# Kernel optimization log

Measured on AMD Instinct MI355X. Metric: run time of the kernel, lower is better.

Reference implementation:

```python
import jax, jax.numpy as jnp
import numpy as np

B, C, T = 32, 64, 512
K = 3            # period_channels / top-k frequencies
PMAX = T         # max period (== seq_len so output matches input length)
MIN_P = 32       # min_period_threshold
CMAX = T // MIN_P  # static upper bound on number of cycles
KERNELS = ((1, 1), (3, 3), (5, 5))


def _conv2d(x, w, b, pad):
    # x: [N, Cin, H, W], w: [Cout, Cin, kh, kw]
    y = jax.lax.conv_general_dilated(
        x, w, (1, 1), ((pad[0], pad[0]), (pad[1], pad[1])),
        dimension_numbers=('NCHW', 'OIHW', 'NCHW'))
    return y + b[None, :, None, None]


def _period_fold(seqs):
    # seqs: [BN, T]. FFT top-k period detection + gather-based fold into 2D grids.
    spec = jnp.fft.rfft(seqs, axis=-1)
    amp = jnp.abs(spec).at[..., 0].set(0.0)  # zero DC component
    vals, idx = jax.lax.top_k(amp, K)        # [BN, K]
    idx = jnp.maximum(idx, 1)
    P = jnp.clip(T // idx, MIN_P, PMAX)      # period length per branch
    cycles = jnp.maximum(T // P, 1)
    base = jnp.maximum(T - cycles * P, 0)    # start offset (keep trailing window)
    idx_c = jnp.arange(CMAX)
    idx_p = jnp.arange(PMAX)
    gidx = (base[:, :, None, None]
            + idx_c[None, None, :, None] * P[:, :, None, None]
            + idx_p[None, None, None, :])
    gidx = jnp.clip(gidx, 0, T - 1)          # [BN, K, CMAX, PMAX]
    gathered = seqs[jnp.arange(seqs.shape[0])[:, None, None, None], gidx]
    mask = ((idx_c[None, None, :, None] < cycles[:, :, None, None])
            & (idx_p[None, None, None, :] < P[:, :, None, None])).astype(seqs.dtype)
    return gathered * mask, mask, vals


def _forward(features, w_path0, b_path0, w_path1, b_path1, w_path2, b_path2,
             w_proj, b_proj, w_res, b_res, w_fuse, b_fuse):
    seqs = features.reshape(B * C, T)
    conv_in, mask, kamp = _period_fold(seqs)  # [B*C, K, CMAX, PMAX]
    # Inception block: parallel same-padded convs + 1x1 proj + residual 1x1 proj
    ws = (w_path0, w_path1, w_path2)
    bs = (b_path0, b_path1, b_path2)
    feats = [_conv2d(conv_in, w, b, (kh // 2, kw // 2))
             for w, b, (kh, kw) in zip(ws, bs, KERNELS)]
    z = _conv2d(jnp.concatenate(feats, axis=1), w_proj, b_proj, (0, 0))
    z = jax.nn.gelu(z, approximate=False)  # torch nn.GELU default = exact erf
    z2d = (z + _conv2d(conv_in, w_res, b_res, (0, 0))).reshape(B, C, CMAX, PMAX)
    mask5 = mask.reshape(B, C, K, CMAX, PMAX)
    conv_in5 = conv_in.reshape(B, C, K, CMAX, PMAX)
    eps = jnp.finfo(z2d.dtype).eps
    neg = jnp.finfo(z2d.dtype).min
    # masked avg / max pooling over cycles
    cycle_mask = mask5.max(axis=2)                       # [B,C,CMAX,PMAX]
    avg_pool = (z2d * cycle_mask).sum(axis=2) / (cycle_mask.sum(axis=2) + eps)
    valid = cycle_mask > 0
    max_pool = jnp.where(valid, z2d, neg).max(axis=2)
    max_pool = jnp.where(valid.any(axis=2), max_pool, 0.0)  # [B,C,PMAX]
    # amplitude-softmax weighted branch reconstruction back to 1D
    branch_sum = conv_in5.sum(axis=3)                    # [B,C,K,PMAX]
    branch_w = mask5.sum(axis=3)
    branch_recon = branch_sum / (branch_w + eps) * (branch_w > 0)
    branch_valid = mask5.max(axis=(3, 4)) > 0            # [B,C,K]
    amp = jnp.where(branch_valid, kamp.reshape(B, C, K), neg)
    bw = jax.nn.softmax(amp, axis=2) * branch_valid
    seq_recon = (branch_recon * bw[..., None]).sum(axis=2)  # [B,C,PMAX]
    combined = jnp.concatenate([avg_pool, max_pool, seq_recon], axis=1)  # [B,3C,PMAX]
    fused = jnp.einsum('oc,bct->bot', w_fuse, combined) + b_fuse[None, :, None]
    return jax.nn.gelu(fused, approximate=False)  # [B, C, T] residual update


def setup_inputs() -> dict:
    key = jax.random.key(0)
    ks = jax.random.split(key, 8)

    def conv_w(k, shape):
        fan_in = shape[1] * shape[2] * shape[3]
        return jax.random.normal(k, shape, jnp.float32) / float(np.sqrt(fan_in))

    inp = {'features': jax.random.normal(ks[0], (B, C, T), jnp.float32)}
    for i, (kh, kw) in enumerate(KERNELS):
        inp[f'w_path{i}'] = conv_w(ks[1 + i], (1, K, kh, kw))
        inp[f'b_path{i}'] = jnp.zeros((1,), jnp.float32)
    inp['w_proj'] = conv_w(ks[4], (1, len(KERNELS), 1, 1))
    inp['b_proj'] = jnp.zeros((1,), jnp.float32)
    inp['w_res'] = conv_w(ks[5], (1, K, 1, 1))
    inp['b_res'] = jnp.zeros((1,), jnp.float32)
    inp['w_fuse'] = jax.random.normal(ks[6], (C, 3 * C), jnp.float32) / float(np.sqrt(3 * C))
    inp['b_fuse'] = jnp.zeros((C,), jnp.float32)
    return inp


def reference(features, w_path0, b_path0, w_path1, b_path1, w_path2, b_path2,
              w_proj, b_proj, w_res, b_res, w_fuse, b_fuse):
    return _forward(features, w_path0, b_path0, w_path1, b_path1, w_path2, b_path2,
                    w_proj, b_proj, w_res, b_res, w_fuse, b_fuse)
```

## Files before the change

### kernel.cpp

```cpp
#include <hip/hip_runtime.h>
#include <math.h>

#define B_    32
#define C_    64
#define T_    512
#define NROWS (B_ * C_)
#define CMAX_ 16
#define FEPS  1.1920929e-07f

__device__ __forceinline__ float gelu_fast(float x) {
    float y = fmaf(0.044715f * x * x, x, x);
    float e = __builtin_exp2f(-2.3022808f * y);
    return x * __builtin_amdgcn_rcpf(1.0f + e);
}

__global__ __launch_bounds__(128) void mono_kernel(
    const float* __restrict__ feat,
    const float* __restrict__ w0, const float* __restrict__ b0,
    const float* __restrict__ w1, const float* __restrict__ b1,
    const float* __restrict__ w2, const float* __restrict__ b2,
    const float* __restrict__ wpj, const float* __restrict__ bpj,
    const float* __restrict__ wr, const float* __restrict__ br,
    float* __restrict__ avg_out, float* __restrict__ max_out,
    float* __restrict__ seq_out)
{
    __shared__ float rowp[1040];
    __shared__ __align__(16) float2 FA[256];
    __shared__ __align__(16) float2 FB[256];
    __shared__ float WeffS[80];
    __shared__ float wtopS[6];
    __shared__ int   itopS[6];
    __shared__ int   ipS[9];
    __shared__ float bwS[3];

    const int tid = threadIdx.x;
    const int lane = tid & 63;
    const int wv = tid >> 6;
    const int r = blockIdx.x;

    {
        float4 v = reinterpret_cast<const float4*>(feat + (size_t)r * T_)[tid];
        int bi = 2 + tid * 4;
        rowp[bi + 0] = v.x; rowp[bi + 1] = v.y;
        rowp[bi + 2] = v.z; rowp[bi + 3] = v.w;
    }
    for (int i = 514 + tid; i < 1040; i += 128) rowp[i] = 0.f;
    if (tid == 0) { rowp[0] = 0.f; rowp[1] = 0.f; }
    if (tid < 80) {
        int i = tid;
        if (i < 75) {
            int k = i / 25, ij = i % 25, ii = ij / 5, jj = ij % 5;
            float w = wpj[2] * w2[k * 25 + ii * 5 + jj];
            if (ii >= 1 && ii <= 3 && jj >= 1 && jj <= 3)
                w += wpj[1] * w1[k * 9 + (ii - 1) * 3 + (jj - 1)];
            if (ii == 2 && jj == 2) w += wpj[0] * w0[k];
            WeffS[i] = w;
        } else if (i == 75) {
            WeffS[75] = wpj[0] * b0[0] + wpj[1] * b1[0] + wpj[2] * b2[0] + bpj[0];
        } else if (i <= 78) {
            WeffS[i] = wr[i - 76];
        } else {
            WeffS[79] = br[0];
        }
    }
    __syncthreads();

    {
        float2* Fw = FA + (wv << 7);
        #pragma unroll
        for (int n = lane; n < 128; n += 64)
            Fw[n] = make_float2(rowp[2 + 4 * n + 2 * wv], rowp[3 + 4 * n + 2 * wv]);
    }

    {
        float2* src = FA + (wv << 7);
        float2* dst = FB + (wv << 7);
        #pragma unroll
        for (int s = 1; s <= 7; ++s) {
            const int l = 1 << (s - 1);
            const int pl = lane & (l - 1);
            const int i0 = 2 * lane - pl;
            const float rev = (float)pl * (0.5f / (float)l);
            const float cw =  __builtin_amdgcn_cosf(rev);
            const float sw = -__builtin_amdgcn_sinf(rev);
            float2 a = src[lane];
            float2 b = src[lane + 64];
            float tr = cw * b.x - sw * b.y;
            float ti = cw * b.y + sw * b.x;
            dst[i0]     = make_float2(a.x + tr, a.y + ti);
            dst[i0 + l] = make_float2(a.x - tr, a.y - ti);
            float2* tmp = src; src = dst; dst = tmp;
        }
    }
    __syncthreads();

    float v[2]; int id[2];
    {
        const float2* Fe = FB;
        const float2* Fo = FB + 128;
        const int k1 = tid + 1;
        const int a = k1 & 127;
        const int b = (128 - a) & 127;
        float2 Fea = Fe[a], Foa = Fo[a], Feb = Fe[b], Fob = Fo[b];
        const float revw = (float)k1 * (1.0f / 256.0f);
        const float cw =  __builtin_amdgcn_cosf(revw);
        const float sw = -__builtin_amdgcn_sinf(revw);
        float wfr = cw * Foa.x - sw * Foa.y, wfi = cw * Foa.y + sw * Foa.x;
        float cfr = cw * Fob.x + sw * Fob.y, cfi = cw * Fob.y - sw * Fob.x;
        const float revu = (float)k1 * (1.0f / 512.0f);
        const float su = __builtin_amdgcn_sinf(revu);
        const float cu = __builtin_amdgcn_cosf(revu);
        #pragma unroll
        for (int q = 0; q < 2; ++q) {
            const float sgn = q ? -1.f : 1.f;
            float Ax = Fea.x + sgn * wfr, Ay = Fea.y + sgn * wfi;
            float Bx = Feb.x + sgn * cfr, By = Feb.y + sgn * cfi;
            float Er = 0.5f * (Ax + Bx);
            float Ei = 0.5f * (Ay - By);
            float Or = 0.5f * (Ay + By);
            float Oi = 0.5f * (Bx - Ax);
            float cth = q ? -su : cu;
            float sth = q ?  cu : su;
            float Fr = Er + cth * Or + sth * Oi;
            float Fi = Ei + cth * Oi - sth * Or;
            v[q] = sqrtf(Fr * Fr + Fi * Fi);
            id[q] = k1 + 128 * q;
        }
    }

    {
        float vals[3]; int idxs[3];
        #pragma unroll
        for (int kk = 0; kk < 3; ++kk) {
            float bv = v[0]; int bi = id[0];
            if (v[1] > bv || (v[1] == bv && id[1] < bi)) { bv = v[1]; bi = id[1]; }
            #pragma unroll
            for (int off = 32; off >= 1; off >>= 1) {
                float ov = __shfl_xor(bv, off, 64);
                int   oi = __shfl_xor(bi, off, 64);
                if (ov > bv || (ov == bv && oi < bi)) { bv = ov; bi = oi; }
            }
            vals[kk] = bv; idxs[kk] = bi;
            #pragma unroll
            for (int q = 0; q < 2; ++q)
                if (id[q] == bi) v[q] = -1e30f;
        }
        if (lane == 0) {
            #pragma unroll
            for (int kk = 0; kk < 3; ++kk) {
                wtopS[wv * 3 + kk] = vals[kk];
                itopS[wv * 3 + kk] = idxs[kk];
            }
        }
    }
    __syncthreads();
    if (tid == 0) {
        float vv[6]; int ii[6];
        #pragma unroll
        for (int q = 0; q < 6; ++q) { vv[q] = wtopS[q]; ii[q] = itopS[q]; }
        float vals[3]; int idxs[3];
        #pragma unroll
        for (int kk = 0; kk < 3; ++kk) {
            float bv = vv[0]; int bi = ii[0];
            #pragma unroll
            for (int q = 1; q < 6; ++q)
                if (vv[q] > bv || (vv[q] == bv && ii[q] < bi)) { bv = vv[q]; bi = ii[q]; }
            vals[kk] = bv; idxs[kk] = bi;
            #pragma unroll
            for (int q = 0; q < 6; ++q)
                if (ii[q] == bi) vv[q] = -1e30f;
        }
        float m = fmaxf(vals[0], fmaxf(vals[1], vals[2]));
        float e0 = expf(vals[0] - m), e1 = expf(vals[1] - m), e2 = expf(vals[2] - m);
        float inv = 1.0f / (e0 + e1 + e2);
        bwS[0] = e0 * inv; bwS[1] = e1 * inv; bwS[2] = e2 * inv;
        #pragma unroll
        for (int kk = 0; kk < 3; ++kk) {
            int fi = idxs[kk];
            int P = T_ / fi;
            P = P < 32 ? 32 : (P > 512 ? 512 : P);
            int cyc = T_ / P;
            ipS[kk] = P; ipS[3 + kk] = cyc; ipS[6 + kk] = T_ - cyc * P;
        }
    }
    __syncthreads();

    const int P0  = __builtin_amdgcn_readfirstlane(ipS[0]);
    const int P1  = __builtin_amdgcn_readfirstlane(ipS[1]);
    const int P2  = __builtin_amdgcn_readfirstlane(ipS[2]);
    const int cy0 = __builtin_amdgcn_readfirstlane(ipS[3]);
    const int cy1 = __builtin_amdgcn_readfirstlane(ipS[4]);
    const int cy2 = __builtin_amdgcn_readfirstlane(ipS[5]);
    const int bs0 = __builtin_amdgcn_readfirstlane(ipS[6]);
    const int bs1 = __builtin_amdgcn_readfirstlane(ipS[7]);
    const int bs2 = __builtin_amdgcn_readfirstlane(ipS[8]);
    const float bw0 = bwS[0], bw1 = bwS[1], bw2 = bwS[2];
    const float beff = WeffS[75], wr0 = WeffS[76], wr1 = WeffS[77],
                wr2 = WeffS[78], bres = WeffS[79];

    int maxP = P0 > P1 ? P0 : P1; maxP = maxP > P2 ? maxP : P2;
    const int PkA[3]  = {P0, P1, P2};
    const int cykA[3] = {cy0, cy1, cy2};
    const int bskA[3] = {bs0, bs1, bs2};
    const int woff = tid & 64;

    #pragma unroll 1
    for (int pc = 0; pc < T_; pc += 128) {
        const int p = pc + tid;
        const int wb = __builtin_amdgcn_readfirstlane(pc + woff);
        if (wb >= maxP) {
            avg_out[r * T_ + p] = 0.f;
            max_out[r * T_ + p] = 0.f;
            seq_out[r * T_ + p] = 0.f;
            continue;
        }
        int c0 = (P0 > wb) ? cy0 : 0;
        int c1 = (P1 > wb) ? cy1 : 0;
        int c2 = (P2 > wb) ? cy2 : 0;
        int cymax = c0 > c1 ? c0 : c1; cymax = cymax > c2 ? cymax : c2;
        cymax = __builtin_amdgcn_readfirstlane(cymax);

        float zacc[CMAX_];
        #pragma unroll
        for (int i = 0; i < CMAX_; ++i) zacc[i] = beff;

        #pragma unroll 1
        for (int k = 0; k < 3; ++k) {
            const int P = PkA[k];
            if (wb >= P) continue;
            const int cy = cykA[k];
            const int bs = bskA[k];
            float Wk[5][5];
            #pragma unroll
            for (int i = 0; i < 5; ++i)
                #pragma unroll
                for (int j = 0; j < 5; ++j)
                    Wk[i][j] = WeffS[k * 25 + i * 5 + j];
            bool mdw[5];
            #pragma unroll
            for (int dw = -2; dw <= 2; ++dw)
                mdw[dw + 2] = ((unsigned)(p + dw) < (unsigned)P);
            const int base = bs + p;
            #pragma unroll
            for (int g = 0; g < 4; ++g) {
                if (4 * g < cy) {
                    #pragma unroll
                    for (int h4 = 0; h4 < 4; ++h4) {
                        const int hh = 4 * g + h4;
                        const int hoff = (hh < cy) ? 0 : 4096;
                        int a0 = base + hh * P + hoff;
                        a0 = a0 > 1031 ? 1031 : a0;
                        float w[5];
                        #pragma unroll
                        for (int dw = 0; dw < 5; ++dw)
                            w[dw] = mdw[dw] ? rowp[a0 + dw] : 0.f;
                        #pragma unroll
                        for (int dh = -2; dh <= 2; ++dh) {
                            const int cc = hh - dh;
                            if (cc >= 0 && cc < CMAX_) {
                                #pragma unroll
                                for (int dw = 0; dw < 5; ++dw)
                                    zacc[cc] = fmaf(Wk[dh + 2][dw], w[dw], zacc[cc]);
                            }
                        }
                    }
                }
            }
        }

        float avg_num = 0.f, den = 0.f, mx = -3.402823466e38f;
        float s0 = 0.f, s1 = 0.f, s2 = 0.f;
        int anyv = 0;
        const int pl0 = (p < P0), pl1 = (p < P1), pl2 = (p < P2);
        #pragma unroll
        for (int cg = 0; cg < 4; ++cg) {
            if (4 * cg < cymax) {
                #pragma unroll
                for (int c4 = 0; c4 < 4; ++c4) {
                    const int cc = 4 * cg + c4;
                    int m0 = (cc < cy0) & pl0;
                    int m1 = (cc < cy1) & pl1;
                    int m2 = (cc < cy2) & pl2;
                    int a0 = 2 + bs0 + cc * P0 + p; a0 = a0 > 1036 ? 1036 : a0;
                    int a1 = 2 + bs1 + cc * P1 + p; a1 = a1 > 1036 ? 1036 : a1;
                    int a2 = 2 + bs2 + cc * P2 + p; a2 = a2 > 1036 ? 1036 : a2;
                    float x0v = m0 ? rowp[a0] : 0.f;
                    float x1v = m1 ? rowp[a1] : 0.f;
                    float x2v = m2 ? rowp[a2] : 0.f;
                    float res = fmaf(wr0, x0v, fmaf(wr1, x1v, fmaf(wr2, x2v, bres)));
                    float z = gelu_fast(zacc[cc]) + res;
                    s0 += x0v; s1 += x1v; s2 += x2v;
                    int mm = m0 | m1 | m2;
                    float cm = mm ? 1.f : 0.f;
                    avg_num += z * cm;
                    den += cm;
                    mx = mm ? fmaxf(mx, z) : mx;
                    anyv |= mm;
                }
            }
        }
        float avg = avg_num / (den + FEPS);
        float mpool = anyv ? mx : 0.f;

        float seq = 0.f;
        seq = fmaf(bw0, pl0 ? s0 / ((float)cy0 + FEPS) : 0.f, seq);
        seq = fmaf(bw1, pl1 ? s1 / ((float)cy1 + FEPS) : 0.f, seq);
        seq = fmaf(bw2, pl2 ? s2 / ((float)cy2 + FEPS) : 0.f, seq);

        avg_out[r * T_ + p] = avg;
        max_out[r * T_ + p] = mpool;
        seq_out[r * T_ + p] = seq;
    }
}

__global__ __launch_bounds__(256) void fuse_kernel(
    const float* __restrict__ avgb, const float* __restrict__ maxb,
    const float* __restrict__ seqb,
    const float* __restrict__ wf, const float* __restrict__ bfu,
    float* __restrict__ out)
{
    __shared__ float wT[64][70];
    __shared__ float Bt[64][40];
    const int tid = threadIdx.x;
    const int b = blockIdx.y;
    const int tt0 = blockIdx.x * 32;
    const int og = tid >> 3;
    const int tg = tid & 7;
    const int o0 = og * 2;
    const int t0 = tg * 4;

    float acc[2][4];
    #pragma unroll
    for (int i = 0; i < 2; ++i)
        #pragma unroll
        for (int j = 0; j < 4; ++j) acc[i][j] = 0.f;

    const float* srcs[3] = {avgb, maxb, seqb};
    for (int g = 0; g < 3; ++g) {
        const float* __restrict__ src = srcs[g];
        #pragma unroll
        for (int it = 0; it < 2; ++it) {
            int idx = tid + it * 256;
            int c = idx >> 3, t4 = idx & 7;
            float4 vv = reinterpret_cast<const float4*>(
                            &src[(b * 64 + c) * 512 + tt0])[t4];
            *reinterpret_cast<float4*>(&Bt[c][t4 * 4]) = vv;
        }
        #pragma unroll
        for (int it = 0; it < 16; ++it) {
            int i = tid + it * 256;
            int c = i & 63, o = i >> 6;
            wT[c][o] = wf[o * 192 + g * 64 + c];
        }
        __syncthreads();
        for (int c = 0; c < 64; ++c) {
            float2 wv = *reinterpret_cast<const float2*>(&wT[c][o0]);
            float4 bv = *reinterpret_cast<const float4*>(&Bt[c][t0]);
            const float wa[2] = {wv.x, wv.y};
            const float ba[4] = {bv.x, bv.y, bv.z, bv.w};
            #pragma unroll
            for (int i = 0; i < 2; ++i)
                #pragma unroll
                for (int j = 0; j < 4; ++j)
                    acc[i][j] = fmaf(wa[i], ba[j], acc[i][j]);
        }
        __syncthreads();
    }
    #pragma unroll
    for (int i = 0; i < 2; ++i) {
        float bias = bfu[o0 + i];
        float4 o4;
        o4.x = gelu_fast(acc[i][0] + bias);
        o4.y = gelu_fast(acc[i][1] + bias);
        o4.z = gelu_fast(acc[i][2] + bias);
        o4.w = gelu_fast(acc[i][3] + bias);
        *reinterpret_cast<float4*>(
            &out[(b * 64 + (o0 + i)) * 512 + tt0 + t0]) = o4;
    }
}

extern "C" void kernel_launch(void* const* d_in, const int* in_sizes, int n_in,
                              void* d_out, int out_size, void* d_ws, size_t ws_size,
                              hipStream_t stream) {
    const float* feat = (const float*)d_in[0];
    const float* w0  = (const float*)d_in[1];
    const float* b0  = (const float*)d_in[2];
    const float* w1  = (const float*)d_in[3];
    const float* b1  = (const float*)d_in[4];
    const float* w2  = (const float*)d_in[5];
    const float* b2  = (const float*)d_in[6];
    const float* wpj = (const float*)d_in[7];
    const float* bpj = (const float*)d_in[8];
    const float* wr  = (const float*)d_in[9];
    const float* br  = (const float*)d_in[10];
    const float* wf  = (const float*)d_in[11];
    const float* bfu = (const float*)d_in[12];

    float* ws = (float*)d_ws;
    float* avgb = ws;
    float* maxb = ws + (size_t)NROWS * T_;
    float* seqb = ws + 2 * (size_t)NROWS * T_;

    mono_kernel<<<NROWS, 128, 0, stream>>>(feat, w0, b0, w1, b1, w2, b2,
                                           wpj, bpj, wr, br, avgb, maxb, seqb);
    fuse_kernel<<<dim3(16, 32), 256, 0, stream>>>(avgb, maxb, seqb, wf, bfu,
                                                  (float*)d_out);
}
```

Baseline: 41.11 us.

## Restructure fold-conv as flattened shared-memory scatter over valid cycle×period cells

Replaces the per-thread register accumulation over all 16 cycle rows with a pass that flattens the valid (cycle, period) cells across threads and writes conv results into a shared-memory z tile, processed in two 256-wide column windows. When all three branch periods match, the three effective 5x5 kernels are summed into one so a single conv pass runs. The z tile reuses the FFT scratch buffers, and the padded row buffer shrinks. The pooling loop becomes a runtime loop bounded by the actual cycle count. This is meant to cut wasted FMAs on masked cells and register pressure, at the cost of extra barriers, shared-memory traffic and a reciprocal-multiply index division.

```diff
diff --git a/kernel.cpp b/kernel.cpp
--- a/kernel.cpp
+++ b/kernel.cpp
@@ -5,13 +5,52 @@
 #define C_    64
 #define T_    512
 #define NROWS (B_ * C_)
-#define CMAX_ 16
 #define FEPS  1.1920929e-07f
+#define ZSTR  260
 
 __device__ __forceinline__ float gelu_fast(float x) {
     float y = fmaf(0.044715f * x * x, x, x);
     float e = __builtin_exp2f(-2.3022808f * y);
     return x * __builtin_amdgcn_rcpf(1.0f + e);
+}
+
+template<bool ACC>
+__device__ __forceinline__ void conv_pass(
+    const float* __restrict__ rowp, float* __restrict__ zsm,
+    const float Wk[5][5], int P, int cy, int bs,
+    int cyI, int PI, int w, int tid)
+{
+    int PwI = PI - (w << 8);
+    PwI = PwI > 256 ? 256 : PwI;
+    if (PwI <= 0) return;
+    const int n = cyI * PwI;
+    const unsigned M = 0xFFFFFFFFu / (unsigned)PwI + 1u;
+    for (int i = tid; i < n; i += 128) {
+        const int cc  = (int)(((unsigned long long)(unsigned)i * M) >> 32);
+        const int ppw = i - cc * PwI;
+        const int pp  = ppw + (w << 8);
+        const int rb  = bs + cc * P + pp;
+        bool hv[5], qv[5];
+        #pragma unroll
+        for (int d = 0; d < 5; ++d) {
+            hv[d] = (unsigned)(cc + d - 2) < (unsigned)cy;
+            qv[d] = (unsigned)(pp + d - 2) < (unsigned)P;
+        }
+        float acc = 0.f;
+        #pragma unroll
+        for (int dh = 0; dh < 5; ++dh) {
+            const int ra = rb + (dh - 2) * P;
+            #pragma unroll
+            for (int dw = 0; dw < 5; ++dw) {
+                unsigned a = (unsigned)(ra + dw - 2);
+                a = a > 511u ? 511u : a;
+                float val = (hv[dh] && qv[dw]) ? rowp[2 + a] : 0.f;
+                acc = fmaf(Wk[dh][dw], val, acc);
+            }
+        }
+        float* zp = zsm + cc * ZSTR + ppw;
+        if (ACC) *zp += acc; else *zp = acc;
+    }
 }
 
 __global__ __launch_bounds__(128) void mono_kernel(
@@ -24,14 +63,16 @@
     float* __restrict__ avg_out, float* __restrict__ max_out,
     float* __restrict__ seq_out)
 {
-    __shared__ float rowp[1040];
-    __shared__ __align__(16) float2 FA[256];
-    __shared__ __align__(16) float2 FB[256];
+    __shared__ float rowp[520];
     __shared__ float WeffS[80];
     __shared__ float wtopS[6];
     __shared__ int   itopS[6];
     __shared__ int   ipS[9];
     __shared__ float bwS[3];
+    __shared__ __align__(16) float smem_u[16 * ZSTR];
+    float2* FA = reinterpret_cast<float2*>(smem_u);
+    float2* FB = FA + 256;
+    float*  zsm = smem_u;
 
     const int tid = threadIdx.x;
     const int lane = tid & 63;
@@ -44,8 +85,8 @@
         rowp[bi + 0] = v.x; rowp[bi + 1] = v.y;
         rowp[bi + 2] = v.z; rowp[bi + 3] = v.w;
     }
-    for (int i = 514 + tid; i < 1040; i += 128) rowp[i] = 0.f;
-    if (tid == 0) { rowp[0] = 0.f; rowp[1] = 0.f; }
+    if (tid < 2) rowp[tid] = 0.f;
+    if (tid >= 122) rowp[392 + tid] = 0.f;
     if (tid < 80) {
         int i = tid;
         if (i < 75) {
@@ -199,117 +240,99 @@
                 wr2 = WeffS[78], bres = WeffS[79];
 
     int maxP = P0 > P1 ? P0 : P1; maxP = maxP > P2 ? maxP : P2;
+    const bool fastp = (P0 == P1) && (P1 == P2);
     const int PkA[3]  = {P0, P1, P2};
     const int cykA[3] = {cy0, cy1, cy2};
     const int bskA[3] = {bs0, bs1, bs2};
-    const int woff = tid & 64;
+    const size_t rT = (size_t)r * T_;
 
     #pragma unroll 1
-    for (int pc = 0; pc < T_; pc += 128) {
-        const int p = pc + tid;
-        const int wb = __builtin_amdgcn_readfirstlane(pc + woff);
-        if (wb >= maxP) {
-            avg_out[r * T_ + p] = 0.f;
-            max_out[r * T_ + p] = 0.f;
-            seq_out[r * T_ + p] = 0.f;
-            continue;
-        }
-        int c0 = (P0 > wb) ? cy0 : 0;
-        int c1 = (P1 > wb) ? cy1 : 0;
-        int c2 = (P2 > wb) ? cy2 : 0;
-        int cymax = c0 > c1 ? c0 : c1; cymax = cymax > c2 ? cymax : c2;
-        cymax = __builtin_amdgcn_readfirstlane(cymax);
-
-        float zacc[CMAX_];
-        #pragma unroll
-        for (int i = 0; i < CMAX_; ++i) zacc[i] = beff;
+    for (int w = 0; w < 2; ++w) {
+        const int wbase = w << 8;
+        if (wbase < maxP) {
+            if (fastp) {
+                float Wk[5][5];
+                #pragma unroll
+                for (int ij = 0; ij < 25; ++ij)
+                    (&Wk[0][0])[ij] = WeffS[ij] + WeffS[25 + ij] + WeffS[50 + ij];
+                conv_pass<false>(rowp, zsm, Wk, P0, cy0, bs0, cy0, P0, w, tid);
+                __syncthreads();
+            } else {
+                #pragma unroll
+                for (int j = 0; j < 8; ++j) {
+                    int idx = tid + (j << 7);
+                    int cc = idx >> 6, p4 = idx & 63;
+                    *reinterpret_cast<float4*>(zsm + cc * ZSTR + (p4 << 2)) =
+                        make_float4(0.f, 0.f, 0.f, 0.f);
+                }
+                __syncthreads();
+                #pragma unroll 1
+                for (int k = 0; k < 3; ++k) {
+                    float Wk[5][5];
+                    #pragma unroll
+                    for (int ij = 0; ij < 25; ++ij)
+                        (&Wk[0][0])[ij] = WeffS[k * 25 + ij];
+                    const int P = PkA[k], cyk = cykA[k], bsk = bskA[k];
+                    int cyI = cyk + 2; cyI = cyI > 16 ? 16 : cyI;
+                    int PI  = P + 2;   PI  = PI > 512 ? 512 : PI;
+                    conv_pass<true>(rowp, zsm, Wk, P, cyk, bsk, cyI, PI, w, tid);
+                    __syncthreads();
+                }
+            }
+        }
 
         #pragma unroll 1
-        for (int k = 0; k < 3; ++k) {
-            const int P = PkA[k];
-            if (wb >= P) continue;
-            const int cy = cykA[k];
-            const int bs = bskA[k];
-            float Wk[5][5];
-            #pragma unroll
-            for (int i = 0; i < 5; ++i)
-                #pragma unroll
-                for (int j = 0; j < 5; ++j)
-                    Wk[i][j] = WeffS[k * 25 + i * 5 + j];
-            bool mdw[5];
-            #pragma unroll
-            for (int dw = -2; dw <= 2; ++dw)
-                mdw[dw + 2] = ((unsigned)(p + dw) < (unsigned)P);
-            const int base = bs + p;
-            #pragma unroll
-            for (int g = 0; g < 4; ++g) {
-                if (4 * g < cy) {
-                    #pragma unroll
-                    for (int h4 = 0; h4 < 4; ++h4) {
-                        const int hh = 4 * g + h4;
-                        const int hoff = (hh < cy) ? 0 : 4096;
-                        int a0 = base + hh * P + hoff;
-                        a0 = a0 > 1031 ? 1031 : a0;
-                        float w[5];
-                        #pragma unroll
-                        for (int dw = 0; dw < 5; ++dw)
-                            w[dw] = mdw[dw] ? rowp[a0 + dw] : 0.f;
-                        #pragma unroll
-                        for (int dh = -2; dh <= 2; ++dh) {
-                            const int cc = hh - dh;
-                            if (cc >= 0 && cc < CMAX_) {
-                                #pragma unroll
-                                for (int dw = 0; dw < 5; ++dw)
-                                    zacc[cc] = fmaf(Wk[dh + 2][dw], w[dw], zacc[cc]);
-                            }
-                        }
-                    }
-                }
-            }
-        }
-
-        float avg_num = 0.f, den = 0.f, mx = -3.402823466e38f;
-        float s0 = 0.f, s1 = 0.f, s2 = 0.f;
-        int anyv = 0;
-        const int pl0 = (p < P0), pl1 = (p < P1), pl2 = (p < P2);
-        #pragma unroll
-        for (int cg = 0; cg < 4; ++cg) {
-            if (4 * cg < cymax) {
-                #pragma unroll
-                for (int c4 = 0; c4 < 4; ++c4) {
-                    const int cc = 4 * cg + c4;
-                    int m0 = (cc < cy0) & pl0;
-                    int m1 = (cc < cy1) & pl1;
-                    int m2 = (cc < cy2) & pl2;
-                    int a0 = 2 + bs0 + cc * P0 + p; a0 = a0 > 1036 ? 1036 : a0;
-                    int a1 = 2 + bs1 + cc * P1 + p; a1 = a1 > 1036 ? 1036 : a1;
-                    int a2 = 2 + bs2 + cc * P2 + p; a2 = a2 > 1036 ? 1036 : a2;
-                    float x0v = m0 ? rowp[a0] : 0.f;
-                    float x1v = m1 ? rowp[a1] : 0.f;
-                    float x2v = m2 ? rowp[a2] : 0.f;
-                    float res = fmaf(wr0, x0v, fmaf(wr1, x1v, fmaf(wr2, x2v, bres)));
-                    float z = gelu_fast(zacc[cc]) + res;
-                    s0 += x0v; s1 += x1v; s2 += x2v;
-                    int mm = m0 | m1 | m2;
-                    float cm = mm ? 1.f : 0.f;
-                    avg_num += z * cm;
-                    den += cm;
-                    mx = mm ? fmaxf(mx, z) : mx;
-                    anyv |= mm;
-                }
-            }
-        }
-        float avg = avg_num / (den + FEPS);
-        float mpool = anyv ? mx : 0.f;
-
-        float seq = 0.f;
-        seq = fmaf(bw0, pl0 ? s0 / ((float)cy0 + FEPS) : 0.f, seq);
-        seq = fmaf(bw1, pl1 ? s1 / ((float)cy1 + FEPS) : 0.f, seq);
-        seq = fmaf(bw2, pl2 ? s2 / ((float)cy2 + FEPS) : 0.f, seq);
-
-        avg_out[r * T_ + p] = avg;
-        max_out[r * T_ + p] = mpool;
-        seq_out[r * T_ + p] = seq;
+        for (int half = 0; half < 2; ++half) {
+            const int pc = wbase + (half << 7);
+            const int p = pc + tid;
+            if (pc >= maxP) {
+                avg_out[rT + p] = 0.f;
+                max_out[rT + p] = 0.f;
+                seq_out[rT + p] = 0.f;
+                continue;
+            }
+            int c0 = (P0 > pc) ? cy0 : 0;
+            int c1 = (P1 > pc) ? cy1 : 0;
+            int c2 = (P2 > pc) ? cy2 : 0;
+            int cymaxc = c0 > c1 ? c0 : c1; cymaxc = cymaxc > c2 ? cymaxc : c2;
+
+            float avg_num = 0.f, den = 0.f, mx = -3.402823466e38f;
+            float s0 = 0.f, s1 = 0.f, s2 = 0.f;
+            int anyv = 0;
+            const int pl0 = (p < P0), pl1 = (p < P1), pl2 = (p < P2);
+            #pragma unroll 1
+            for (int cc = 0; cc < cymaxc; ++cc) {
+                int m0 = (cc < cy0) & pl0;
+                int m1 = (cc < cy1) & pl1;
+                int m2 = (cc < cy2) & pl2;
+                float zr = zsm[cc * ZSTR + (p - wbase)];
+                unsigned a0 = (unsigned)(bs0 + cc * P0 + p); a0 = a0 > 511u ? 511u : a0;
+                unsigned a1 = (unsigned)(bs1 + cc * P1 + p); a1 = a1 > 511u ? 511u : a1;
+                unsigned a2 = (unsigned)(bs2 + cc * P2 + p); a2 = a2 > 511u ? 511u : a2;
+                float x0v = m0 ? rowp[2 + a0] : 0.f;
+                float x1v = m1 ? rowp[2 + a1] : 0.f;
+                float x2v = m2 ? rowp[2 + a2] : 0.f;
+                float res = fmaf(wr0, x0v, fmaf(wr1, x1v, fmaf(wr2, x2v, bres)));
+                float zv = gelu_fast(zr + beff) + res;
+                int mm = m0 | m1 | m2;
+                avg_num += mm ? zv : 0.f;
+                den     += mm ? 1.f : 0.f;
+                mx = mm ? fmaxf(mx, zv) : mx;
+                anyv |= mm;
+                s0 += x0v; s1 += x1v; s2 += x2v;
+            }
+            float avg = avg_num / (den + FEPS);
+            float mpool = anyv ? mx : 0.f;
+            float seq = 0.f;
+            seq = fmaf(bw0, pl0 ? s0 / ((float)cy0 + FEPS) : 0.f, seq);
+            seq = fmaf(bw1, pl1 ? s1 / ((float)cy1 + FEPS) : 0.f, seq);
+            seq = fmaf(bw2, pl2 ? s2 / ((float)cy2 + FEPS) : 0.f, seq);
+
+            avg_out[rT + p] = avg;
+            max_out[rT + p] = mpool;
+            seq_out[rT + p] = seq;
+        }
+        __syncthreads();
     }
 }
 
```

After: 51.53 us. 25.4% more time.
